# Optimization experiments

Hardware: AMD Instinct MI355X
Metric: run time of the kernel (lower is better)

Reference implementation:

```python
import jax, jax.numpy as jnp
import numpy as np

B, S, D = 32, 2048, 1024
TEMP = 9.0  # RelaxedBernoulli temperature (torch.tensor([9]))


def setup_inputs() -> dict:
    key = jax.random.key(0)
    ks = jax.random.split(key, 12)
    sd = 1.0 / np.sqrt(D)
    sd2 = 1.0 / np.sqrt(2 * D)
    return {
        "h_t": jax.random.normal(ks[0], (B, D), jnp.float32),
        "h_s": jax.random.normal(ks[1], (B, S, D), jnp.float32),
        "auxi_hs": jax.random.normal(ks[2], (B, S, D), jnp.float32),
        "noise_u": jax.random.uniform(ks[3], (B, S, 1), jnp.float32),
        # linear_map: Linear(2*dim, 1) with bias
        "Wmap": jax.random.normal(ks[4], (2 * D,), jnp.float32) * sd2,
        "bmap": jax.random.normal(ks[5], (), jnp.float32) * sd2,
        # mlp_h: Linear(dim, dim) + Tanh + Linear(dim, 1)
        "W1": jax.random.normal(ks[6], (D, D), jnp.float32) * sd,
        "b1": jax.random.normal(ks[7], (D,), jnp.float32) * sd,
        "W2": jax.random.normal(ks[8], (D,), jnp.float32) * sd,
        "b2": jax.random.normal(ks[9], (), jnp.float32) * sd,
        # linear_out: Linear(2*dim, dim, bias=False) (attn_type='dot')
        "Wout": jax.random.normal(ks[10], (D, 2 * D), jnp.float32) * sd2,
    }


def reference(h_t, h_s, auxi_hs, noise_u, Wmap, bmap, W1, b1, W2, b2, Wout):
    # h_t: (B, D) one-step query; h_s, auxi_hs: (B, S, D)
    d = h_s.shape[-1]
    # linear_map(concat(auxi_hs, H_t)) without materializing the (B,S,2D) concat
    Wm_a, Wm_t = Wmap[:d], Wmap[d:]
    logits_p = jnp.einsum('bsd,d->bs', auxi_hs, Wm_a) + (h_t @ Wm_t)[:, None] + bmap  # (B,S)
    logits_p = logits_p[..., None]  # (B,S,1); note logit(sigmoid(x)) == x
    # RelaxedBernoulli(temp=9, probs=sigmoid(logits_p)).sample() with explicit uniform noise
    eps = 1e-7
    u = jnp.clip(noise_u, eps, 1.0 - eps)
    logistic = jnp.log(u) - jnp.log1p(-u)  # (B,S,1)
    G = jax.nn.sigmoid((logits_p + logistic) / TEMP)  # (B,S,1)
    # mlp_h(h_s): Linear -> tanh -> Linear
    e = jnp.einsum('bsd,d->bs', jnp.tanh(jnp.einsum('bsd,ed->bse', h_s, W1) + b1), W2) + b2
    e = e[..., None]  # (B,S,1)
    # custom softmax: max over dim 0 (batch!), exp, gate
    v = jnp.max(e, axis=0, keepdims=True)  # (1,S,1)
    scores = jnp.exp(e - v) * G  # (B,S,1)
    align = scores[..., 0] / jnp.sum(scores[..., 0], axis=1, keepdims=True)  # (B,S)
    c = jnp.einsum('bs,bsd->bd', align, h_s)  # (B,D)
    attn_h = jnp.tanh(jnp.concatenate([c, h_t], axis=-1) @ Wout.T)  # (B,D)
    return attn_h, align
```

## Files before the change

kernel.cpp:

```cpp
#include <hip/hip_runtime.h>
#include <hip/hip_bf16.h>
#include <math.h>

#define B_ 32
#define S_ 2048
#define D_ 1024
#define TEMP_ 9.0f

typedef __attribute__((ext_vector_type(8))) short short8;
typedef __attribute__((ext_vector_type(4))) float f32x4;
typedef __attribute__((ext_vector_type(4))) unsigned short ushort4v;

__device__ __forceinline__ unsigned short f2b(float f) {
  union { float f; unsigned int u; } v; v.f = f;
  unsigned int r = v.u;
  r += 0x7fffu + ((r >> 16) & 1u);
  return (unsigned short)(r >> 16);
}
__device__ __forceinline__ float b2f(unsigned short b) {
  union { float f; unsigned int u; } v; v.u = ((unsigned int)b) << 16;
  return v.f;
}
__device__ __forceinline__ float tanh_fast(float x) {
  float ez = __expf(2.f * x);
  return 1.f - __fdividef(2.f, ez + 1.f);
}

#define GLOAD_LDS16(g, l) \
  __builtin_amdgcn_global_load_lds((const __attribute__((address_space(1))) void*)(g), \
                                   (__attribute__((address_space(3))) void*)(l), 16, 0, 0)

__global__ void k_conv(const float* __restrict__ src, unsigned short* __restrict__ dst, int n8) {
  int i = blockIdx.x * 256 + threadIdx.x;
  if (i >= n8) return;
  const float4* g = reinterpret_cast<const float4*>(src) + (size_t)i * 2;
  float4 x0 = g[0], x1 = g[1];
  uint4 w;
  w.x = f2b(x0.x) | ((unsigned)f2b(x0.y) << 16);
  w.y = f2b(x0.z) | ((unsigned)f2b(x0.w) << 16);
  w.z = f2b(x1.x) | ((unsigned)f2b(x1.y) << 16);
  w.w = f2b(x1.z) | ((unsigned)f2b(x1.w) << 16);
  reinterpret_cast<uint4*>(dst)[i] = w;
}

__global__ void k0_tdot(const float* __restrict__ h_t, const float* __restrict__ Wmap,
                        const float* __restrict__ bmap, float* __restrict__ tdot) {
  int b = blockIdx.x;
  int t = threadIdx.x;
  float p = 0.f;
  for (int k = t; k < D_; k += 256) p += h_t[b*D_ + k] * Wmap[D_ + k];
  __shared__ float red[256];
  red[t] = p; __syncthreads();
  for (int off = 128; off > 0; off >>= 1) { if (t < off) red[t] += red[t+off]; __syncthreads(); }
  if (t == 0) tdot[b] = red[0] + bmap[0];
}

__global__ void k1_gate(const float* __restrict__ aux, const float* __restrict__ Wmap,
                        const float* __restrict__ noise, const float* __restrict__ tdot,
                        float* __restrict__ Gout) {
  int w = (blockIdx.x * 256 + threadIdx.x) >> 6;
  int lane = threadIdx.x & 63;
  const float4* arow = reinterpret_cast<const float4*>(aux + (size_t)w * D_);
  const float4* wrow = reinterpret_cast<const float4*>(Wmap);
  float p = 0.f;
  for (int it = 0; it < 4; ++it) {
    float4 a = arow[it*64 + lane];
    float4 m = wrow[it*64 + lane];
    p += a.x*m.x + a.y*m.y + a.z*m.z + a.w*m.w;
  }
  for (int msk = 32; msk > 0; msk >>= 1) p += __shfl_xor(p, msk);
  if (lane == 0) {
    int b = w >> 11;
    float logits = p + tdot[b];
    float u = noise[w];
    u = fminf(fmaxf(u, 1e-7f), 1.f - 1e-7f);
    float logistic = logf(u) - log1pf(-u);
    float x = (logits + logistic) / TEMP_;
    Gout[w] = 1.f / (1.f + expf(-x));
  }
}

#define BK3 32
#define NT3 (D_ / BK3)

extern __shared__ unsigned short lds2[];

__global__ __launch_bounds__(512, 2) void k2_pipe(
    const unsigned short* __restrict__ Ag, const unsigned short* __restrict__ Bg,
    const float* __restrict__ b1, const float* __restrict__ W2,
    float* __restrict__ e_buf) {
  int hw = blockIdx.x;
  int xcd = hw & 7;
  int sub = hw >> 3;
  int cc  = sub & 3;
  int rc  = xcd + 8 * (sub >> 2);
  int rowBase = rc * 256;
  int colBase = cc * 256;

  int t = threadIdx.x;
  int lane = t & 63;
  int wv = t >> 6;
  int wr = wv >> 2, wc = wv & 3;
  int kslot = lane >> 4;

  f32x4 acc[8][4] = {};

  auto stage = [&](int tt) {
    unsigned short* dstA = lds2 + (tt & 3) * 16384;
    unsigned short* dstB = dstA + 8192;
    int k0 = tt * BK3;
#pragma unroll
    for (int i = 0; i < 2; ++i) {
      int c = i * 512 + t;
      int r = c >> 2;
      int clog = (c & 3) ^ ((r >> 1) & 3);
      GLOAD_LDS16(Ag + (size_t)(rowBase + r) * D_ + k0 + clog * 8, (char*)dstA + c * 16);
    }
#pragma unroll
    for (int i = 0; i < 2; ++i) {
      int c = i * 512 + t;
      int r = c >> 2;
      int clog = (c & 3) ^ ((r >> 1) & 3);
      GLOAD_LDS16(Bg + (size_t)(colBase + r) * D_ + k0 + clog * 8, (char*)dstB + c * 16);
    }
  };

#define K2_TILE(T, VM, DO_STAGE) do {                                          \
    asm volatile("s_waitcnt lgkmcnt(0)\n\ts_waitcnt vmcnt(" #VM ")" ::: "memory"); \
    __builtin_amdgcn_s_barrier();                                              \
    __builtin_amdgcn_sched_barrier(0);                                         \
    const unsigned short* Ab = lds2 + ((T) & 3) * 16384;                       \
    const unsigned short* Bb = Ab + 8192;                                      \
    short8 af[8], bf[4];                                                       \
    _Pragma("unroll")                                                          \
    for (int m = 0; m < 8; ++m) {                                              \
      int r = wr * 128 + m * 16 + (lane & 15);                                 \
      int byte = r * 64 + ((kslot ^ ((r >> 1) & 3)) << 4);                     \
      af[m] = *reinterpret_cast<const short8*>(                                \
          reinterpret_cast<const char*>(Ab) + byte);                           \
    }                                                                          \
    _Pragma("unroll")                                                          \
    for (int n = 0; n < 4; ++n) {                                              \
      int r = wc * 64 + n * 16 + (lane & 15);                                  \
      int byte = r * 64 + ((kslot ^ ((r >> 1) & 3)) << 4);                     \
      bf[n] = *reinterpret_cast<const short8*>(                                \
          reinterpret_cast<const char*>(Bb) + byte);                           \
    }                                                                          \
    if (DO_STAGE) stage((T) + 3);                                              \
    __builtin_amdgcn_s_setprio(1);                                             \
    _Pragma("unroll")                                                          \
    for (int m = 0; m < 8; ++m)                                                \
      _Pragma("unroll")                                                        \
      for (int n = 0; n < 4; ++n)                                              \
        acc[m][n] = __builtin_amdgcn_mfma_f32_16x16x32_bf16(af[m], bf[n], acc[m][n], 0, 0, 0); \
    __builtin_amdgcn_s_setprio(0);                                             \
  } while (0)

  stage(0); stage(1); stage(2);
  for (int tt = 0; tt <= NT3 - 4; ++tt) K2_TILE(tt, 8, true);
  K2_TILE(NT3 - 3, 8, false);
  K2_TILE(NT3 - 2, 4, false);
  K2_TILE(NT3 - 1, 0, false);
#undef K2_TILE

  float b1v[4], w2v[4];
#pragma unroll
  for (int n = 0; n < 4; ++n) {
    int col = colBase + wc * 64 + n * 16 + (lane & 15);
    b1v[n] = b1[col];
    w2v[n] = W2[col];
  }
#pragma unroll
  for (int m = 0; m < 8; ++m) {
#pragma unroll
    for (int j = 0; j < 4; ++j) {
      float s = 0.f;
#pragma unroll
      for (int n = 0; n < 4; ++n)
        s += tanh_fast(acc[m][n][j] + b1v[n]) * w2v[n];
      s += __shfl_xor(s, 1);
      s += __shfl_xor(s, 2);
      s += __shfl_xor(s, 4);
      s += __shfl_xor(s, 8);
      if ((lane & 15) == 0) {
        int row = rowBase + wr * 128 + m * 16 + ((lane >> 4) << 2) + j;
        atomicAdd(&e_buf[row], s);
      }
    }
  }
}

#define BM 128
#define BN 128
#define BK 64
__global__ __launch_bounds__(256) void k2_egemm_f32(
    const float* __restrict__ h_s, const float* __restrict__ W1,
    const float* __restrict__ b1, const float* __restrict__ W2,
    float* __restrict__ e_buf) {
  __shared__ unsigned short As[BM * BK];
  __shared__ unsigned short Bs[BN * BK];
  int bid = blockIdx.x;
  int colBase = (bid & 7) * BN;
  int rowBase = (bid >> 3) * BM;
  int t = threadIdx.x;
  int lane = t & 63;
  int wave = t >> 6;
  int wr = wave >> 1, wc = wave & 1;
  f32x4 acc[4][4] = {};
  for (int k0 = 0; k0 < D_; k0 += BK) {
    __syncthreads();
    for (int i = 0; i < 4; ++i) {
      int flat = i*256 + t;
      int r = flat >> 3;
      int c8 = flat & 7;
      int byte = (r*128 + c8*16) ^ ((r & 7) << 4);
      {
        const float4* g = reinterpret_cast<const float4*>(h_s + (size_t)(rowBase + r)*D_ + k0 + c8*8);
        float4 x0 = g[0], x1 = g[1];
        uint4 w;
        w.x = f2b(x0.x) | ((unsigned)f2b(x0.y) << 16);
        w.y = f2b(x0.z) | ((unsigned)f2b(x0.w) << 16);
        w.z = f2b(x1.x) | ((unsigned)f2b(x1.y) << 16);
        w.w = f2b(x1.z) | ((unsigned)f2b(x1.w) << 16);
        *reinterpret_cast<uint4*>(reinterpret_cast<char*>(As) + byte) = w;
      }
      {
        const float4* g = reinterpret_cast<const float4*>(W1 + (size_t)(colBase + r)*D_ + k0 + c8*8);
        float4 x0 = g[0], x1 = g[1];
        uint4 w;
        w.x = f2b(x0.x) | ((unsigned)f2b(x0.y) << 16);
        w.y = f2b(x0.z) | ((unsigned)f2b(x0.w) << 16);
        w.z = f2b(x1.x) | ((unsigned)f2b(x1.y) << 16);
        w.w = f2b(x1.z) | ((unsigned)f2b(x1.w) << 16);
        *reinterpret_cast<uint4*>(reinterpret_cast<char*>(Bs) + byte) = w;
      }
    }
    __syncthreads();
    for (int kk = 0; kk < BK; kk += 32) {
      short8 af[4], bf[4];
      int kByte = kk*2 + ((lane >> 4) << 4);
      for (int m = 0; m < 4; ++m) {
        int r = wr*64 + m*16 + (lane & 15);
        int byte = (r*128 + kByte) ^ ((r & 7) << 4);
        af[m] = *reinterpret_cast<const short8*>(reinterpret_cast<const char*>(As) + byte);
      }
      for (int n = 0; n < 4; ++n) {
        int r = wc*64 + n*16 + (lane & 15);
        int byte = (r*128 + kByte) ^ ((r & 7) << 4);
        bf[n] = *reinterpret_cast<const short8*>(reinterpret_cast<const char*>(Bs) + byte);
      }
      for (int m = 0; m < 4; ++m)
        for (int n = 0; n < 4; ++n)
          acc[m][n] = __builtin_amdgcn_mfma_f32_16x16x32_bf16(af[m], bf[n], acc[m][n], 0, 0, 0);
    }
  }
  float b1v[4], w2v[4];
  for (int n = 0; n < 4; ++n) {
    int col = colBase + wc*64 + n*16 + (lane & 15);
    b1v[n] = b1[col];
    w2v[n] = W2[col];
  }
  for (int m = 0; m < 4; ++m) {
    for (int j = 0; j < 4; ++j) {
      float s = 0.f;
      for (int n = 0; n < 4; ++n)
        s += tanhf(acc[m][n][j] + b1v[n]) * w2v[n];
      s += __shfl_xor(s, 1);
      s += __shfl_xor(s, 2);
      s += __shfl_xor(s, 4);
      s += __shfl_xor(s, 8);
      if ((lane & 15) == 0) {
        int row = rowBase + wr*64 + m*16 + ((lane >> 4) << 2) + j;
        atomicAdd(&e_buf[row], s);
      }
    }
  }
}

__global__ void k3a_vmax(const float* __restrict__ e_buf, float* __restrict__ v) {
  int s = blockIdx.x * 256 + threadIdx.x;
  if (s >= S_) return;
  float m = -1e30f;
  for (int b = 0; b < B_; ++b) m = fmaxf(m, e_buf[b*S_ + s]);
  v[s] = m;
}

__global__ void k3b_align(const float* __restrict__ e_buf, const float* __restrict__ v,
                          float* __restrict__ galign) {
  int b = blockIdx.x;
  int t = threadIdx.x;
  __shared__ float sc[S_];
  __shared__ float red[256];
  float p = 0.f;
  for (int s = t; s < S_; s += 256) {
    float x = expf(e_buf[b*S_ + s] - v[s]) * galign[b*S_ + s];
    sc[s] = x;
    p += x;
  }
  red[t] = p; __syncthreads();
  for (int off = 128; off > 0; off >>= 1) { if (t < off) red[t] += red[t+off]; __syncthreads(); }
  float inv = 1.f / red[0];
  for (int s = t; s < S_; s += 256) galign[b*S_ + s] = sc[s] * inv;
}

__global__ void k4_ctx_bf16(const unsigned short* __restrict__ hsb, const float* __restrict__ align,
                            float* __restrict__ c) {
  int bid = blockIdx.x;
  int b = bid >> 6;
  int sBase = (bid & 63) * 32;
  int t = threadIdx.x;
  float4 accv = {0.f, 0.f, 0.f, 0.f};
  for (int si = 0; si < 32; ++si) {
    int s = sBase + si;
    float a = align[b*S_ + s];
    ushort4v hv = *reinterpret_cast<const ushort4v*>(hsb + (size_t)(b*S_ + s)*D_ + t*4);
    accv.x += a*b2f(hv.x); accv.y += a*b2f(hv.y); accv.z += a*b2f(hv.z); accv.w += a*b2f(hv.w);
  }
  atomicAdd(&c[b*D_ + t*4 + 0], accv.x);
  atomicAdd(&c[b*D_ + t*4 + 1], accv.y);
  atomicAdd(&c[b*D_ + t*4 + 2], accv.z);
  atomicAdd(&c[b*D_ + t*4 + 3], accv.w);
}

__global__ void k4_ctx_f32(const float* __restrict__ h_s, const float* __restrict__ align,
                           float* __restrict__ c) {
  int bid = blockIdx.x;
  int b = bid >> 6;
  int sBase = (bid & 63) * 32;
  int t = threadIdx.x;
  float4 accv = {0.f, 0.f, 0.f, 0.f};
  for (int si = 0; si < 32; ++si) {
    int s = sBase + si;
    float a = align[b*S_ + s];
    float4 hv = *reinterpret_cast<const float4*>(h_s + (size_t)(b*S_ + s)*D_ + t*4);
    accv.x += a*hv.x; accv.y += a*hv.y; accv.z += a*hv.z; accv.w += a*hv.w;
  }
  atomicAdd(&c[b*D_ + t*4 + 0], accv.x);
  atomicAdd(&c[b*D_ + t*4 + 1], accv.y);
  atomicAdd(&c[b*D_ + t*4 + 2], accv.z);
  atomicAdd(&c[b*D_ + t*4 + 3], accv.w);
}

__global__ void k5_out(const float* __restrict__ c, const float* __restrict__ h_t,
                       const float* __restrict__ Wout, float* __restrict__ out) {
  int W = (blockIdx.x * 256 + threadIdx.x) >> 6;
  int lane = threadIdx.x & 63;
  int b = W >> 10;
  int o = W & 1023;
  const float* wrow = Wout + (size_t)o * (2 * D_);
  float p = 0.f;
  for (int it = 0; it < 16; ++it) {
    int k = it*64 + lane;
    p += c[b*D_ + k] * wrow[k];
  }
  for (int it = 16; it < 32; ++it) {
    int k = it*64 + lane;
    p += h_t[b*D_ + (k - D_)] * wrow[k];
  }
  for (int m = 32; m > 0; m >>= 1) p += __shfl_xor(p, m);
  if (lane == 0) out[b*D_ + o] = tanhf(p);
}

extern "C" void kernel_launch(void* const* d_in, const int* in_sizes, int n_in,
                              void* d_out, int out_size, void* d_ws, size_t ws_size,
                              hipStream_t stream) {
  const float* h_t   = (const float*)d_in[0];
  const float* h_s   = (const float*)d_in[1];
  const float* aux   = (const float*)d_in[2];
  const float* noise = (const float*)d_in[3];
  const float* Wmap  = (const float*)d_in[4];
  const float* bmap  = (const float*)d_in[5];
  const float* W1    = (const float*)d_in[6];
  const float* b1    = (const float*)d_in[7];
  const float* W2    = (const float*)d_in[8];
  const float* Wout  = (const float*)d_in[10];

  float* out    = (float*)d_out;
  float* galign = out + B_*D_;

  const size_t HS_N   = (size_t)B_*S_*D_;
  const size_t W1_N   = (size_t)D_*D_;
  const size_t needed = HS_N*2 + W1_N*2 + (65536 + 32 + 2048 + 32768) * sizeof(float);

  if (ws_size >= needed) {
    unsigned short* hs_bf = (unsigned short*)d_ws;
    unsigned short* w1_bf = hs_bf + HS_N;
    float* fws   = (float*)(w1_bf + W1_N);
    float* e_buf = fws;
    float* tdot  = fws + 65536;
    float* v     = fws + 65568;
    float* c     = fws + 67616;

    hipMemsetAsync(e_buf, 0, 65536 * sizeof(float), stream);
    hipMemsetAsync(c, 0, 32768 * sizeof(float), stream);

    hipFuncSetAttribute(reinterpret_cast<const void*>(k2_pipe),
                        hipFuncAttributeMaxDynamicSharedMemorySize, 131072);

    k_conv<<<(int)(HS_N/8/256), 256, 0, stream>>>(h_s, hs_bf, (int)(HS_N/8));
    k_conv<<<(int)(W1_N/8/256), 256, 0, stream>>>(W1, w1_bf, (int)(W1_N/8));
    k0_tdot<<<32, 256, 0, stream>>>(h_t, Wmap, bmap, tdot);
    k1_gate<<<16384, 256, 0, stream>>>(aux, Wmap, noise, tdot, galign);
    k2_pipe<<<1024, 512, 131072, stream>>>(hs_bf, w1_bf, b1, W2, e_buf);
    k3a_vmax<<<8, 256, 0, stream>>>(e_buf, v);
    k3b_align<<<32, 256, 0, stream>>>(e_buf, v, galign);
    k4_ctx_bf16<<<2048, 256, 0, stream>>>(hs_bf, galign, c);
    k5_out<<<8192, 256, 0, stream>>>(c, h_t, Wout, out);
  } else {
    float* ws    = (float*)d_ws;
    float* e_buf = ws;
    float* tdot  = ws + 65536;
    float* v     = ws + 65568;
    float* c     = ws + 67616;

    hipMemsetAsync(e_buf, 0, 65536 * sizeof(float), stream);
    hipMemsetAsync(c, 0, 32768 * sizeof(float), stream);

    k0_tdot<<<32, 256, 0, stream>>>(h_t, Wmap, bmap, tdot);
    k1_gate<<<16384, 256, 0, stream>>>(aux, Wmap, noise, tdot, galign);
    k2_egemm_f32<<<4096, 256, 0, stream>>>(h_s, W1, b1, W2, e_buf);
    k3a_vmax<<<8, 256, 0, stream>>>(e_buf, v);
    k3b_align<<<32, 256, 0, stream>>>(e_buf, v, galign);
    k4_ctx_f32<<<2048, 256, 0, stream>>>(h_s, galign, c);
    k5_out<<<8192, 256, 0, stream>>>(c, h_t, Wout, out);
  }
}
```

Measured before the change: 364.7 us.

## Hoist LDS/global offsets, issue prefetch early, interleave A-fragment loads with MFMAs

The mlp_h GEMM main loop now precomputes swizzled LDS read offsets and global source pointers once per thread instead of every tile. It issues the global-to-LDS prefetch for tile T+3 right after the barrier, rather than after the fragment reads. It also loads the A fragments in two halves, each followed by its MFMAs, so LDS reads overlap matrix math. The loop is fully unrolled and the sched_barrier is dropped, which cuts integer work and gives the scheduler more freedom, at the cost of more code size and possibly more register pressure.

```diff
diff --git a/kernel.cpp b/kernel.cpp
--- a/kernel.cpp
+++ b/kernel.cpp
@@ -103,65 +103,79 @@
   int wr = wv >> 2, wc = wv & 3;
   int kslot = lane >> 4;
 
+  int aOff[8], bOff[4];
+#pragma unroll
+  for (int m = 0; m < 8; ++m) {
+    int ra = wr * 128 + m * 16 + (lane & 15);
+    aOff[m] = ra * 64 + ((kslot ^ ((ra >> 1) & 3)) << 4);
+  }
+#pragma unroll
+  for (int n = 0; n < 4; ++n) {
+    int rb = wc * 64 + n * 16 + (lane & 15);
+    bOff[n] = 16384 + rb * 64 + ((kslot ^ ((rb >> 1) & 3)) << 4);
+  }
+
+  const unsigned short* gA[2];
+  const unsigned short* gB[2];
+  int dstOff[2];
+#pragma unroll
+  for (int i = 0; i < 2; ++i) {
+    int c = i * 512 + t;
+    int r = c >> 2;
+    int clog = (c & 3) ^ ((r >> 1) & 3);
+    gA[i] = Ag + (size_t)(rowBase + r) * D_ + clog * 8;
+    gB[i] = Bg + (size_t)(colBase + r) * D_ + clog * 8;
+    dstOff[i] = c * 16;
+  }
+
   f32x4 acc[8][4] = {};
 
-  auto stage = [&](int tt) {
-    unsigned short* dstA = lds2 + (tt & 3) * 16384;
-    unsigned short* dstB = dstA + 8192;
-    int k0 = tt * BK3;
-#pragma unroll
-    for (int i = 0; i < 2; ++i) {
-      int c = i * 512 + t;
-      int r = c >> 2;
-      int clog = (c & 3) ^ ((r >> 1) & 3);
-      GLOAD_LDS16(Ag + (size_t)(rowBase + r) * D_ + k0 + clog * 8, (char*)dstA + c * 16);
-    }
-#pragma unroll
-    for (int i = 0; i < 2; ++i) {
-      int c = i * 512 + t;
-      int r = c >> 2;
-      int clog = (c & 3) ^ ((r >> 1) & 3);
-      GLOAD_LDS16(Bg + (size_t)(colBase + r) * D_ + k0 + clog * 8, (char*)dstB + c * 16);
-    }
-  };
+#define STAGE(TT) do {                                                         \
+    char* _ba = (char*)lds2 + ((TT) & 3) * 32768;                              \
+    GLOAD_LDS16(gA[0] + (TT) * 32, _ba + dstOff[0]);                           \
+    GLOAD_LDS16(gA[1] + (TT) * 32, _ba + dstOff[1]);                           \
+    GLOAD_LDS16(gB[0] + (TT) * 32, _ba + 16384 + dstOff[0]);                   \
+    GLOAD_LDS16(gB[1] + (TT) * 32, _ba + 16384 + dstOff[1]);                   \
+  } while (0)
 
 #define K2_TILE(T, VM, DO_STAGE) do {                                          \
     asm volatile("s_waitcnt lgkmcnt(0)\n\ts_waitcnt vmcnt(" #VM ")" ::: "memory"); \
     __builtin_amdgcn_s_barrier();                                              \
-    __builtin_amdgcn_sched_barrier(0);                                         \
-    const unsigned short* Ab = lds2 + ((T) & 3) * 16384;                       \
-    const unsigned short* Bb = Ab + 8192;                                      \
+    if (DO_STAGE) STAGE((T) + 3);                                              \
+    const char* _ab = (const char*)lds2 + ((T) & 3) * 32768;                   \
     short8 af[8], bf[4];                                                       \
     _Pragma("unroll")                                                          \
-    for (int m = 0; m < 8; ++m) {                                              \
-      int r = wr * 128 + m * 16 + (lane & 15);                                 \
-      int byte = r * 64 + ((kslot ^ ((r >> 1) & 3)) << 4);                     \
-      af[m] = *reinterpret_cast<const short8*>(                                \
-          reinterpret_cast<const char*>(Ab) + byte);                           \
-    }                                                                          \
+    for (int n = 0; n < 4; ++n)                                                \
+      bf[n] = *reinterpret_cast<const short8*>(_ab + bOff[n]);                 \
     _Pragma("unroll")                                                          \
-    for (int n = 0; n < 4; ++n) {                                              \
-      int r = wc * 64 + n * 16 + (lane & 15);                                  \
-      int byte = r * 64 + ((kslot ^ ((r >> 1) & 3)) << 4);                     \
-      bf[n] = *reinterpret_cast<const short8*>(                                \
-          reinterpret_cast<const char*>(Bb) + byte);                           \
-    }                                                                          \
-    if (DO_STAGE) stage((T) + 3);                                              \
+    for (int m = 0; m < 4; ++m)                                                \
+      af[m] = *reinterpret_cast<const short8*>(_ab + aOff[m]);                 \
     __builtin_amdgcn_s_setprio(1);                                             \
     _Pragma("unroll")                                                          \
-    for (int m = 0; m < 8; ++m)                                                \
+    for (int m = 0; m < 4; ++m)                                                \
+      _Pragma("unroll")                                                        \
+      for (int n = 0; n < 4; ++n)                                              \
+        acc[m][n] = __builtin_amdgcn_mfma_f32_16x16x32_bf16(af[m], bf[n], acc[m][n], 0, 0, 0); \
+    _Pragma("unroll")                                                          \
+    for (int m = 4; m < 8; ++m)                                                \
+      af[m] = *reinterpret_cast<const short8*>(_ab + aOff[m]);                 \
+    _Pragma("unroll")                                                          \
+    for (int m = 4; m < 8; ++m)                                                \
       _Pragma("unroll")                                                        \
       for (int n = 0; n < 4; ++n)                                              \
         acc[m][n] = __builtin_amdgcn_mfma_f32_16x16x32_bf16(af[m], bf[n], acc[m][n], 0, 0, 0); \
     __builtin_amdgcn_s_setprio(0);                                             \
   } while (0)
 
-  stage(0); stage(1); stage(2);
-  for (int tt = 0; tt <= NT3 - 4; ++tt) K2_TILE(tt, 8, true);
-  K2_TILE(NT3 - 3, 8, false);
-  K2_TILE(NT3 - 2, 4, false);
-  K2_TILE(NT3 - 1, 0, false);
+  STAGE(0); STAGE(1); STAGE(2);
+#pragma unroll
+  for (int tt = 0; tt < 28; ++tt) K2_TILE(tt, 8, true);
+  K2_TILE(28, 8, true);
+  K2_TILE(29, 8, false);
+  K2_TILE(30, 4, false);
+  K2_TILE(31, 0, false);
 #undef K2_TILE
+#undef STAGE
 
   float b1v[4], w2v[4];
 #pragma unroll
```

After: 362.3 us. Within noise of the previous version (-0.7%).
